# Optimization experiments

Measured on AMD Instinct MI355X. Metric: run time of the kernel, lower is better.

The kernel has to match this reference:

```python
import jax, jax.numpy as jnp
import numpy as np

B, S, D, H, DH = 2, 2048, 1024, 16, 64  # batch, seq, d_hidden, n_head, d_head


def setup_inputs() -> dict:
    key = jax.random.key(0)
    ks = jax.random.split(key, 11)
    sc = 0.02
    inp = {
        "Q": jax.random.normal(ks[0], (B, S, D), jnp.float32),
        "K": jax.random.normal(ks[1], (B, S, D), jnp.float32),
        "V": jax.random.normal(ks[2], (B, S, D), jnp.float32),
        # causal mask: True = masked (strictly upper triangular), broadcast to [B,S,S]
        "attn_mask": jnp.broadcast_to(jnp.triu(jnp.ones((S, S), bool), k=1), (B, S, S)),
        "W_q": jax.random.normal(ks[3], (H * DH, D), jnp.float32) * sc,
        "b_q": jnp.zeros((H * DH,), jnp.float32),
        "W_k": jax.random.normal(ks[4], (H * DH, D), jnp.float32) * sc,
        "b_k": jnp.zeros((H * DH,), jnp.float32),
        "W_v": jax.random.normal(ks[5], (H * DH, D), jnp.float32) * sc,
        "b_v": jnp.zeros((H * DH,), jnp.float32),
        "W_o": jax.random.normal(ks[6], (D, H * DH), jnp.float32) * sc,
        "b_o": jnp.zeros((D,), jnp.float32),
    }
    return inp


def reference(Q, K, V, attn_mask, W_q, b_q, W_k, b_k, W_v, b_v, W_o, b_o):
    scaler = 1.0 / (DH ** 0.5)
    # projections: torch Linear is x @ W.T + b
    def proj(x, W, b):
        y = jnp.einsum('bsd,ed->bse', x, W) + b  # e = H*DH
        return y.reshape(x.shape[0], x.shape[1], H, DH).transpose(0, 2, 1, 3)  # [B,H,S,DH]
    q = proj(Q, W_q, b_q)
    k = proj(K, W_k, b_k)
    v = proj(V, W_v, b_v)
    score = jnp.einsum('bhqd,bhkd->bhqk', q, k) * scaler
    score = jnp.where(attn_mask[:, None, :, :], jnp.float32(-1e9), score)
    attn_prob = jax.nn.softmax(score, axis=-1)  # dropout p=0.0 -> identity
    context = jnp.einsum('bhqk,bhkd->bhqd', attn_prob, v)
    context = context.transpose(0, 2, 1, 3).reshape(Q.shape[0], -1, H * DH)
    output = jnp.einsum('bse,de->bsd', context, W_o) + b_o
    return (output, attn_prob)
```

## Files before the change

kernel.cpp:

```cpp
#include <hip/hip_runtime.h>
#include <hip/hip_bf16.h>

typedef __attribute__((ext_vector_type(8))) __bf16 bf16x8;
typedef __attribute__((ext_vector_type(4))) float f32x4;
typedef __attribute__((ext_vector_type(4))) unsigned int u32x4;
typedef __attribute__((ext_vector_type(4))) float f4;

#define MB 2
#define MS 2048
#define MD 1024
#define MH 16
#define MDH 64

__device__ __forceinline__ void cvt_store16(const float* __restrict__ src, __bf16* dst) {
  f4 f0 = *(const f4*)src;
  f4 f1 = *(const f4*)(src + 4);
  f4 f2 = *(const f4*)(src + 8);
  f4 f3 = *(const f4*)(src + 12);
  bf16x8 lo, hi;
#pragma unroll
  for (int j = 0; j < 4; j++) {
    lo[j]     = (__bf16)f0[j];
    lo[j + 4] = (__bf16)f1[j];
    hi[j]     = (__bf16)f2[j];
    hi[j + 4] = (__bf16)f3[j];
  }
  *(bf16x8*)dst = lo;
  *(bf16x8*)(dst + 8) = hi;
}

template <bool ABF16>
__device__ __forceinline__ void gemm_core(const void* __restrict__ Aptr,
                                          const float* __restrict__ W,
                                          int tile_m, int tile_n,
                                          f32x4 acc[4][4]) {
  constexpr int LDT = 40;
  __shared__ __bf16 a_lds[128 * LDT];
  __shared__ __bf16 w_lds[128 * LDT];
  const int t = threadIdx.x;
  const int lane = t & 63;
  const int wave = t >> 6;
  const int l15 = lane & 15;
  const int quad = lane >> 4;
  const int wr = wave >> 1;
  const int wc = wave & 1;
  const int srow = t >> 1;
  const int scol = (t & 1) * 16;

  const f32x4 fzero = {0.f, 0.f, 0.f, 0.f};
#pragma unroll
  for (int mi = 0; mi < 4; mi++)
#pragma unroll
    for (int ni = 0; ni < 4; ni++) acc[mi][ni] = fzero;

  for (int k0 = 0; k0 < 1024; k0 += 32) {
    __syncthreads();
    if (ABF16) {
      const __bf16* A = (const __bf16*)Aptr;
      const __bf16* src = A + (size_t)(tile_m * 128 + srow) * 1024 + k0 + scol;
      u32x4 d0 = *(const u32x4*)src;
      u32x4 d1 = *(const u32x4*)(src + 8);
      *(u32x4*)&a_lds[srow * LDT + scol] = d0;
      *(u32x4*)&a_lds[srow * LDT + scol + 8] = d1;
    } else {
      const float* A = (const float*)Aptr;
      cvt_store16(A + (size_t)(tile_m * 128 + srow) * 1024 + k0 + scol,
                  &a_lds[srow * LDT + scol]);
    }
    cvt_store16(W + (size_t)(tile_n * 128 + srow) * 1024 + k0 + scol,
                &w_lds[srow * LDT + scol]);
    __syncthreads();

    bf16x8 af[4], bfr[4];
#pragma unroll
    for (int mi = 0; mi < 4; mi++)
      af[mi] = *(const bf16x8*)&a_lds[(wr * 64 + mi * 16 + l15) * LDT + quad * 8];
#pragma unroll
    for (int ni = 0; ni < 4; ni++)
      bfr[ni] = *(const bf16x8*)&w_lds[(wc * 64 + ni * 16 + l15) * LDT + quad * 8];
#pragma unroll
    for (int mi = 0; mi < 4; mi++)
#pragma unroll
      for (int ni = 0; ni < 4; ni++)
        acc[mi][ni] = __builtin_amdgcn_mfma_f32_16x16x32_bf16(af[mi], bfr[ni], acc[mi][ni], 0, 0, 0);
  }
}

__global__ __launch_bounds__(256) void qkv_proj(
    const float* __restrict__ Q, const float* __restrict__ K, const float* __restrict__ V,
    const float* __restrict__ Wq, const float* __restrict__ Wk, const float* __restrict__ Wv,
    const float* __restrict__ bq, const float* __restrict__ bk, const float* __restrict__ bv,
    __bf16* __restrict__ qo, __bf16* __restrict__ ko, __bf16* __restrict__ vo) {
  const int z = blockIdx.z;
  const float* A = (z == 0) ? Q : ((z == 1) ? K : V);
  const float* W = (z == 0) ? Wq : ((z == 1) ? Wk : Wv);
  const float* bias = (z == 0) ? bq : ((z == 1) ? bk : bv);
  __bf16* out = (z == 0) ? qo : ((z == 1) ? ko : vo);

  f32x4 acc[4][4];
  gemm_core<false>(A, W, blockIdx.y, blockIdx.x, acc);

  const int t = threadIdx.x;
  const int lane = t & 63, wave = t >> 6;
  const int l15 = lane & 15, quad = lane >> 4;
  const int wr = wave >> 1, wc = wave & 1;
  const float scale = (z == 0) ? 0.125f : 1.0f;

#pragma unroll
  for (int ni = 0; ni < 4; ni++) {
    const int e = blockIdx.x * 128 + wc * 64 + ni * 16 + l15;
    const float bias_v = bias[e];
    const int h = e >> 6, dh = e & 63;
#pragma unroll
    for (int mi = 0; mi < 4; mi++) {
#pragma unroll
      for (int r = 0; r < 4; r++) {
        const int sg = blockIdx.y * 128 + wr * 64 + mi * 16 + quad * 4 + r;
        const int bb = sg >> 11, s = sg & 2047;
        const float val = (acc[mi][ni][r] + bias_v) * scale;
        size_t addr;
        if (z < 2) addr = ((size_t)((bb * 16 + h) * 2048 + s)) * 64 + dh;
        else       addr = ((size_t)((bb * 16 + h) * 64 + dh)) * 2048 + s;
        out[addr] = (__bf16)val;
      }
    }
  }
}

__global__ __launch_bounds__(256) void attn_kernel(
    const __bf16* __restrict__ q, const __bf16* __restrict__ k,
    const __bf16* __restrict__ vt, float* __restrict__ P, __bf16* __restrict__ ctx) {
  const int qt = blockIdx.x, h = blockIdx.y, b = blockIdx.z;
  const int bh = b * 16 + h;
  const int t = threadIdx.x;
  const int lane = t & 63, wave = t >> 6;
  const int l15 = lane & 15, quad = lane >> 4;
  const int q0 = qt * 64;

  __shared__ __bf16 q_lds[64 * 72];
  __shared__ __bf16 k_lds[64 * 72];
  __shared__ __bf16 v_lds[64 * 72];
  __shared__ __bf16 p_lds[4 * 16 * 72];

  const __bf16* qbase = q + ((size_t)bh * 2048 + q0) * 64;
  const __bf16* kbase = k + (size_t)bh * 2048 * 64;
  const __bf16* vbase = vt + (size_t)bh * 64 * 2048;
  float* Pbase = P + ((size_t)bh * 2048 + q0) * 2048;

#pragma unroll
  for (int i = 0; i < 2; i++) {
    const int idx = t + i * 256;
    const int row = idx >> 3, c8 = (idx & 7) * 8;
    *(u32x4*)&q_lds[row * 72 + c8] = *(const u32x4*)(qbase + row * 64 + c8);
  }
  __syncthreads();
  bf16x8 qf[2];
  qf[0] = *(const bf16x8*)&q_lds[(wave * 16 + l15) * 72 + quad * 8];
  qf[1] = *(const bf16x8*)&q_lds[(wave * 16 + l15) * 72 + 32 + quad * 8];

  float m[4], l[4];
#pragma unroll
  for (int r = 0; r < 4; r++) { m[r] = -1e30f; l[r] = 0.f; }

  const f32x4 fzero = {0.f, 0.f, 0.f, 0.f};

  for (int kt = 0; kt <= qt; kt++) {
    __syncthreads();
#pragma unroll
    for (int i = 0; i < 2; i++) {
      const int idx = t + i * 256;
      const int row = idx >> 3, c8 = (idx & 7) * 8;
      *(u32x4*)&k_lds[row * 72 + c8] =
          *(const u32x4*)(kbase + (size_t)(kt * 64 + row) * 64 + c8);
    }
    __syncthreads();

    f32x4 sc[4];
#pragma unroll
    for (int blk = 0; blk < 4; blk++) {
      bf16x8 kf0 = *(const bf16x8*)&k_lds[(blk * 16 + l15) * 72 + quad * 8];
      bf16x8 kf1 = *(const bf16x8*)&k_lds[(blk * 16 + l15) * 72 + 32 + quad * 8];
      f32x4 zz = fzero;
      zz = __builtin_amdgcn_mfma_f32_16x16x32_bf16(qf[0], kf0, zz, 0, 0, 0);
      zz = __builtin_amdgcn_mfma_f32_16x16x32_bf16(qf[1], kf1, zz, 0, 0, 0);
      sc[blk] = zz;
    }
#pragma unroll
    for (int r = 0; r < 4; r++) {
      const int qrow = q0 + wave * 16 + quad * 4 + r;
      float sv[4];
      float rowmax = -1e30f;
#pragma unroll
      for (int blk = 0; blk < 4; blk++) {
        const int kcol = kt * 64 + blk * 16 + l15;
        float s = sc[blk][r];
        s = (kcol > qrow) ? -1e30f : s;
        sv[blk] = s;
        rowmax = fmaxf(rowmax, s);
      }
#pragma unroll
      for (int msk = 1; msk < 16; msk <<= 1)
        rowmax = fmaxf(rowmax, __shfl_xor(rowmax, msk, 64));
      const float mnew = fmaxf(m[r], rowmax);
      float se = 0.f;
#pragma unroll
      for (int blk = 0; blk < 4; blk++) se += __expf(sv[blk] - mnew);
#pragma unroll
      for (int msk = 1; msk < 16; msk <<= 1) se += __shfl_xor(se, msk, 64);
      l[r] = l[r] * __expf(m[r] - mnew) + se;
      m[r] = mnew;
    }
  }

  float rl[4];
#pragma unroll
  for (int r = 0; r < 4; r++) rl[r] = 1.0f / l[r];

  f32x4 o[4];
#pragma unroll
  for (int dblk = 0; dblk < 4; dblk++) o[dblk] = fzero;

  for (int kt = 0; kt < 32; kt++) {
    if (kt <= qt) {
      __syncthreads();
#pragma unroll
      for (int i = 0; i < 2; i++) {
        const int idx = t + i * 256;
        const int row = idx >> 3, c8 = (idx & 7) * 8;
        *(u32x4*)&k_lds[row * 72 + c8] =
            *(const u32x4*)(kbase + (size_t)(kt * 64 + row) * 64 + c8);
        *(u32x4*)&v_lds[row * 72 + c8] =
            *(const u32x4*)(vbase + (size_t)row * 2048 + kt * 64 + c8);
      }
      __syncthreads();

      f32x4 sc[4];
#pragma unroll
      for (int blk = 0; blk < 4; blk++) {
        bf16x8 kf0 = *(const bf16x8*)&k_lds[(blk * 16 + l15) * 72 + quad * 8];
        bf16x8 kf1 = *(const bf16x8*)&k_lds[(blk * 16 + l15) * 72 + 32 + quad * 8];
        f32x4 zz = fzero;
        zz = __builtin_amdgcn_mfma_f32_16x16x32_bf16(qf[0], kf0, zz, 0, 0, 0);
        zz = __builtin_amdgcn_mfma_f32_16x16x32_bf16(qf[1], kf1, zz, 0, 0, 0);
        sc[blk] = zz;
      }
#pragma unroll
      for (int r = 0; r < 4; r++) {
        const int qrow = q0 + wave * 16 + quad * 4 + r;
#pragma unroll
        for (int blk = 0; blk < 4; blk++) {
          const int kcol = kt * 64 + blk * 16 + l15;
          float s = sc[blk][r];
          s = (kcol > qrow) ? -1e30f : s;
          const float p = __expf(s - m[r]) * rl[r];
          Pbase[(size_t)(wave * 16 + quad * 4 + r) * 2048 + kcol] = p;
          p_lds[(wave * 16 + quad * 4 + r) * 72 + blk * 16 + l15] = (__bf16)p;
        }
      }
      bf16x8 pf0 = *(const bf16x8*)&p_lds[(wave * 16 + l15) * 72 + quad * 8];
      bf16x8 pf1 = *(const bf16x8*)&p_lds[(wave * 16 + l15) * 72 + 32 + quad * 8];
#pragma unroll
      for (int dblk = 0; dblk < 4; dblk++) {
        bf16x8 vf0 = *(const bf16x8*)&v_lds[(dblk * 16 + l15) * 72 + quad * 8];
        bf16x8 vf1 = *(const bf16x8*)&v_lds[(dblk * 16 + l15) * 72 + 32 + quad * 8];
        o[dblk] = __builtin_amdgcn_mfma_f32_16x16x32_bf16(pf0, vf0, o[dblk], 0, 0, 0);
        o[dblk] = __builtin_amdgcn_mfma_f32_16x16x32_bf16(pf1, vf1, o[dblk], 0, 0, 0);
      }
    } else {
#pragma unroll
      for (int r = 0; r < 4; r++)
#pragma unroll
        for (int blk = 0; blk < 4; blk++)
          Pbase[(size_t)(wave * 16 + quad * 4 + r) * 2048 + kt * 64 + blk * 16 + l15] = 0.f;
    }
  }

#pragma unroll
  for (int dblk = 0; dblk < 4; dblk++) {
#pragma unroll
    for (int r = 0; r < 4; r++) {
      const int sl = wave * 16 + quad * 4 + r;
      const size_t idx = ((size_t)(b * 2048 + q0 + sl)) * 1024 + h * 64 + dblk * 16 + l15;
      ctx[idx] = (__bf16)o[dblk][r];
    }
  }
}

__global__ __launch_bounds__(256) void out_proj(
    const __bf16* __restrict__ ctxp, const float* __restrict__ Wo,
    const float* __restrict__ bo, float* __restrict__ out) {
  f32x4 acc[4][4];
  gemm_core<true>(ctxp, Wo, blockIdx.y, blockIdx.x, acc);

  const int t = threadIdx.x;
  const int lane = t & 63, wave = t >> 6;
  const int l15 = lane & 15, quad = lane >> 4;
  const int wr = wave >> 1, wc = wave & 1;

#pragma unroll
  for (int ni = 0; ni < 4; ni++) {
    const int e = blockIdx.x * 128 + wc * 64 + ni * 16 + l15;
    const float bias_v = bo[e];
#pragma unroll
    for (int mi = 0; mi < 4; mi++) {
#pragma unroll
      for (int r = 0; r < 4; r++) {
        const int sg = blockIdx.y * 128 + wr * 64 + mi * 16 + quad * 4 + r;
        out[(size_t)sg * 1024 + e] = acc[mi][ni][r] + bias_v;
      }
    }
  }
}

extern "C" void kernel_launch(void* const* d_in, const int* in_sizes, int n_in,
                              void* d_out, int out_size, void* d_ws, size_t ws_size,
                              hipStream_t stream) {
  const float* Q  = (const float*)d_in[0];
  const float* K  = (const float*)d_in[1];
  const float* V  = (const float*)d_in[2];
  const float* Wq = (const float*)d_in[4];
  const float* bq = (const float*)d_in[5];
  const float* Wk = (const float*)d_in[6];
  const float* bk = (const float*)d_in[7];
  const float* Wv = (const float*)d_in[8];
  const float* bv = (const float*)d_in[9];
  const float* Wo = (const float*)d_in[10];
  const float* bo = (const float*)d_in[11];

  float* out0 = (float*)d_out;
  float* P = out0 + (size_t)MB * MS * MD;

  __bf16* qws = (__bf16*)d_ws;
  __bf16* kws = qws + (size_t)4194304;
  __bf16* vws = kws + (size_t)4194304;
  __bf16* cws = vws + (size_t)4194304;

  qkv_proj<<<dim3(8, 32, 3), 256, 0, stream>>>(Q, K, V, Wq, Wk, Wv, bq, bk, bv,
                                               qws, kws, vws);
  attn_kernel<<<dim3(32, 16, 2), 256, 0, stream>>>(qws, kws, vws, P, cws);
  out_proj<<<dim3(8, 32, 1), 256, 0, stream>>>(cws, Wo, bo, out0);
}
```

Measured before the change: 867.7 us.

## Pre-convert inputs to bf16, use direct global-to-LDS loads, restructure attention passes

Adds a separate kernel that converts Q/K/V and all weights to bf16 up front, so the GEMMs can stage tiles with global_load_lds into XOR-swizzled LDS using K=64 steps. The attention kernel's first pass now keeps per-lane running max/sum and merges across lanes only once at the end, processing two K tiles per sync. The masked upper region of P is zero-filled with vectorized stores instead of a per-tile loop. Query tiles are also launched heaviest-first to balance the causal work. The cost is an extra launch plus an extra round trip through memory for the converted activations, and more workspace.

Result: faster. 772.8 us (-10.9%).

```diff
diff --git a/kernel.cpp b/kernel.cpp
--- a/kernel.cpp
+++ b/kernel.cpp
@@ -3,7 +3,6 @@
 
 typedef __attribute__((ext_vector_type(8))) __bf16 bf16x8;
 typedef __attribute__((ext_vector_type(4))) float f32x4;
-typedef __attribute__((ext_vector_type(4))) unsigned int u32x4;
 typedef __attribute__((ext_vector_type(4))) float f4;
 
 #define MB 2
@@ -12,40 +11,69 @@
 #define MH 16
 #define MDH 64
 
-__device__ __forceinline__ void cvt_store16(const float* __restrict__ src, __bf16* dst) {
-  f4 f0 = *(const f4*)src;
-  f4 f1 = *(const f4*)(src + 4);
-  f4 f2 = *(const f4*)(src + 8);
-  f4 f3 = *(const f4*)(src + 12);
-  bf16x8 lo, hi;
+__device__ __forceinline__ void gl_lds16(const __bf16* g, __bf16* l) {
+  __builtin_amdgcn_global_load_lds(
+      (const __attribute__((address_space(1))) unsigned int*)g,
+      (__attribute__((address_space(3))) unsigned int*)l, 16, 0, 0);
+}
+
+__device__ __forceinline__ void stage64(const __bf16* __restrict__ g, int gstride,
+                                        __bf16* lds, int t) {
+#pragma unroll
+  for (int j = 0; j < 2; j++) {
+    const int slot = t + j * 256;
+    const int r = slot >> 3;
+    const int c = (slot & 7) ^ (r & 7);
+    gl_lds16(g + (size_t)r * gstride + c * 8, &lds[slot * 8]);
+  }
+}
+
+__device__ __forceinline__ bf16x8 frag_ld(const __bf16* lds, int row, int kc) {
+  const int slot = row * 8 + (kc ^ (row & 7));
+  return *(const bf16x8*)&lds[slot * 8];
+}
+
+__global__ __launch_bounds__(256) void convert_kernel(
+    const float* __restrict__ Q, const float* __restrict__ K, const float* __restrict__ V,
+    const float* __restrict__ Wq, const float* __restrict__ Wk, const float* __restrict__ Wv,
+    const float* __restrict__ Wo, __bf16* __restrict__ Ab, __bf16* __restrict__ Wb) {
+  const size_t base = ((size_t)blockIdx.x * 256 + threadIdx.x) * 8;
+  const float* src;
+  __bf16* dst;
+  size_t off;
+  if (base < 3UL * 4194304UL) {
+    const int z = (int)(base >> 22);
+    off = base & 4194303UL;
+    src = (z == 0) ? Q : ((z == 1) ? K : V);
+    dst = Ab + ((size_t)z << 22);
+  } else {
+    const size_t b2 = base - 3UL * 4194304UL;
+    const int w = (int)(b2 >> 20);
+    off = b2 & 1048575UL;
+    src = (w == 0) ? Wq : ((w == 1) ? Wk : ((w == 2) ? Wv : Wo));
+    dst = Wb + ((size_t)w << 20);
+  }
+  f4 a = *(const f4*)(src + off);
+  f4 b = *(const f4*)(src + off + 4);
+  bf16x8 o;
 #pragma unroll
   for (int j = 0; j < 4; j++) {
-    lo[j]     = (__bf16)f0[j];
-    lo[j + 4] = (__bf16)f1[j];
-    hi[j]     = (__bf16)f2[j];
-    hi[j + 4] = (__bf16)f3[j];
-  }
-  *(bf16x8*)dst = lo;
-  *(bf16x8*)(dst + 8) = hi;
-}
-
-template <bool ABF16>
-__device__ __forceinline__ void gemm_core(const void* __restrict__ Aptr,
-                                          const float* __restrict__ W,
+    o[j] = (__bf16)a[j];
+    o[j + 4] = (__bf16)b[j];
+  }
+  *(bf16x8*)(dst + off) = o;
+}
+
+__device__ __forceinline__ void gemm_core(const __bf16* __restrict__ A,
+                                          const __bf16* __restrict__ W,
                                           int tile_m, int tile_n,
                                           f32x4 acc[4][4]) {
-  constexpr int LDT = 40;
-  __shared__ __bf16 a_lds[128 * LDT];
-  __shared__ __bf16 w_lds[128 * LDT];
+  __shared__ __bf16 a_lds[8192];
+  __shared__ __bf16 w_lds[8192];
   const int t = threadIdx.x;
-  const int lane = t & 63;
-  const int wave = t >> 6;
-  const int l15 = lane & 15;
-  const int quad = lane >> 4;
-  const int wr = wave >> 1;
-  const int wc = wave & 1;
-  const int srow = t >> 1;
-  const int scol = (t & 1) * 16;
+  const int lane = t & 63, wave = t >> 6;
+  const int l15 = lane & 15, quad = lane >> 4;
+  const int wr = wave >> 1, wc = wave & 1;
 
   const f32x4 fzero = {0.f, 0.f, 0.f, 0.f};
 #pragma unroll
@@ -53,52 +81,57 @@
 #pragma unroll
     for (int ni = 0; ni < 4; ni++) acc[mi][ni] = fzero;
 
-  for (int k0 = 0; k0 < 1024; k0 += 32) {
-    __syncthreads();
-    if (ABF16) {
-      const __bf16* A = (const __bf16*)Aptr;
-      const __bf16* src = A + (size_t)(tile_m * 128 + srow) * 1024 + k0 + scol;
-      u32x4 d0 = *(const u32x4*)src;
-      u32x4 d1 = *(const u32x4*)(src + 8);
-      *(u32x4*)&a_lds[srow * LDT + scol] = d0;
-      *(u32x4*)&a_lds[srow * LDT + scol + 8] = d1;
-    } else {
-      const float* A = (const float*)Aptr;
-      cvt_store16(A + (size_t)(tile_m * 128 + srow) * 1024 + k0 + scol,
-                  &a_lds[srow * LDT + scol]);
-    }
-    cvt_store16(W + (size_t)(tile_n * 128 + srow) * 1024 + k0 + scol,
-                &w_lds[srow * LDT + scol]);
-    __syncthreads();
-
-    bf16x8 af[4], bfr[4];
-#pragma unroll
-    for (int mi = 0; mi < 4; mi++)
-      af[mi] = *(const bf16x8*)&a_lds[(wr * 64 + mi * 16 + l15) * LDT + quad * 8];
-#pragma unroll
-    for (int ni = 0; ni < 4; ni++)
-      bfr[ni] = *(const bf16x8*)&w_lds[(wc * 64 + ni * 16 + l15) * LDT + quad * 8];
-#pragma unroll
-    for (int mi = 0; mi < 4; mi++)
+  const __bf16* Abase = A + (size_t)(tile_m * 128) * 1024;
+  const __bf16* Wbase = W + (size_t)(tile_n * 128) * 1024;
+
+  for (int k0 = 0; k0 < 1024; k0 += 64) {
+    __syncthreads();
+#pragma unroll
+    for (int j = 0; j < 4; j++) {
+      const int slot = t + j * 256;
+      const int r = slot >> 3;
+      const int c = (slot & 7) ^ (r & 7);
+      gl_lds16(Abase + (size_t)r * 1024 + k0 + c * 8, &a_lds[slot * 8]);
+    }
+#pragma unroll
+    for (int j = 0; j < 4; j++) {
+      const int slot = t + j * 256;
+      const int r = slot >> 3;
+      const int c = (slot & 7) ^ (r & 7);
+      gl_lds16(Wbase + (size_t)r * 1024 + k0 + c * 8, &w_lds[slot * 8]);
+    }
+    __syncthreads();
+
+#pragma unroll
+    for (int kk = 0; kk < 2; kk++) {
+      bf16x8 af[4], bf[4];
+#pragma unroll
+      for (int mi = 0; mi < 4; mi++)
+        af[mi] = frag_ld(a_lds, wr * 64 + mi * 16 + l15, kk * 4 + quad);
 #pragma unroll
       for (int ni = 0; ni < 4; ni++)
-        acc[mi][ni] = __builtin_amdgcn_mfma_f32_16x16x32_bf16(af[mi], bfr[ni], acc[mi][ni], 0, 0, 0);
+        bf[ni] = frag_ld(w_lds, wc * 64 + ni * 16 + l15, kk * 4 + quad);
+#pragma unroll
+      for (int mi = 0; mi < 4; mi++)
+#pragma unroll
+        for (int ni = 0; ni < 4; ni++)
+          acc[mi][ni] = __builtin_amdgcn_mfma_f32_16x16x32_bf16(af[mi], bf[ni], acc[mi][ni], 0, 0, 0);
+    }
   }
 }
 
 __global__ __launch_bounds__(256) void qkv_proj(
-    const float* __restrict__ Q, const float* __restrict__ K, const float* __restrict__ V,
-    const float* __restrict__ Wq, const float* __restrict__ Wk, const float* __restrict__ Wv,
+    const __bf16* __restrict__ Ab, const __bf16* __restrict__ Wb,
     const float* __restrict__ bq, const float* __restrict__ bk, const float* __restrict__ bv,
     __bf16* __restrict__ qo, __bf16* __restrict__ ko, __bf16* __restrict__ vo) {
   const int z = blockIdx.z;
-  const float* A = (z == 0) ? Q : ((z == 1) ? K : V);
-  const float* W = (z == 0) ? Wq : ((z == 1) ? Wk : Wv);
+  const __bf16* A = Ab + ((size_t)z << 22);
+  const __bf16* W = Wb + ((size_t)z << 20);
   const float* bias = (z == 0) ? bq : ((z == 1) ? bk : bv);
   __bf16* out = (z == 0) ? qo : ((z == 1) ? ko : vo);
 
   f32x4 acc[4][4];
-  gemm_core<false>(A, W, blockIdx.y, blockIdx.x, acc);
+  gemm_core(A, W, blockIdx.y, blockIdx.x, acc);
 
   const int t = threadIdx.x;
   const int lane = t & 63, wave = t >> 6;
@@ -127,19 +160,57 @@
   }
 }
 
+__device__ __forceinline__ void qk_tile(const __bf16* kl, const bf16x8 qf0, const bf16x8 qf1,
+                                        int l15, int quad, f32x4 sc[4]) {
+  const f32x4 fzero = {0.f, 0.f, 0.f, 0.f};
+#pragma unroll
+  for (int blk = 0; blk < 4; blk++) {
+    bf16x8 kf0 = frag_ld(kl, blk * 16 + l15, quad);
+    bf16x8 kf1 = frag_ld(kl, blk * 16 + l15, 4 + quad);
+    f32x4 z = fzero;
+    z = __builtin_amdgcn_mfma_f32_16x16x32_bf16(qf0, kf0, z, 0, 0, 0);
+    z = __builtin_amdgcn_mfma_f32_16x16x32_bf16(qf1, kf1, z, 0, 0, 0);
+    sc[blk] = z;
+  }
+}
+
+__device__ __forceinline__ void sm_update(const f32x4 sc[4], int kt, int q0, int wave,
+                                          int quad, int l15, float m[4], float l[4]) {
+#pragma unroll
+  for (int r = 0; r < 4; r++) {
+    const int qrow = q0 + wave * 16 + quad * 4 + r;
+    float sv[4];
+    float nm = m[r];
+#pragma unroll
+    for (int blk = 0; blk < 4; blk++) {
+      const int kcol = kt * 64 + blk * 16 + l15;
+      float s = sc[blk][r];
+      s = (kcol > qrow) ? -1e30f : s;
+      sv[blk] = s;
+      nm = fmaxf(nm, s);
+    }
+    float acc = l[r] * __expf(m[r] - nm);
+#pragma unroll
+    for (int blk = 0; blk < 4; blk++) acc += __expf(sv[blk] - nm);
+    l[r] = acc;
+    m[r] = nm;
+  }
+}
+
 __global__ __launch_bounds__(256) void attn_kernel(
     const __bf16* __restrict__ q, const __bf16* __restrict__ k,
     const __bf16* __restrict__ vt, float* __restrict__ P, __bf16* __restrict__ ctx) {
-  const int qt = blockIdx.x, h = blockIdx.y, b = blockIdx.z;
+  const int qt = 31 - blockIdx.x;
+  const int h = blockIdx.y, b = blockIdx.z;
   const int bh = b * 16 + h;
   const int t = threadIdx.x;
   const int lane = t & 63, wave = t >> 6;
   const int l15 = lane & 15, quad = lane >> 4;
   const int q0 = qt * 64;
 
-  __shared__ __bf16 q_lds[64 * 72];
-  __shared__ __bf16 k_lds[64 * 72];
-  __shared__ __bf16 v_lds[64 * 72];
+  __shared__ __bf16 q_lds[4096];
+  __shared__ __bf16 k_lds[4096];
+  __shared__ __bf16 v_lds[4096];
   __shared__ __bf16 p_lds[4 * 16 * 72];
 
   const __bf16* qbase = q + ((size_t)bh * 2048 + q0) * 64;
@@ -147,150 +218,105 @@
   const __bf16* vbase = vt + (size_t)bh * 64 * 2048;
   float* Pbase = P + ((size_t)bh * 2048 + q0) * 2048;
 
-#pragma unroll
-  for (int i = 0; i < 2; i++) {
-    const int idx = t + i * 256;
-    const int row = idx >> 3, c8 = (idx & 7) * 8;
-    *(u32x4*)&q_lds[row * 72 + c8] = *(const u32x4*)(qbase + row * 64 + c8);
-  }
+  stage64(qbase, 64, q_lds, t);
   __syncthreads();
-  bf16x8 qf[2];
-  qf[0] = *(const bf16x8*)&q_lds[(wave * 16 + l15) * 72 + quad * 8];
-  qf[1] = *(const bf16x8*)&q_lds[(wave * 16 + l15) * 72 + 32 + quad * 8];
+  const bf16x8 qf0 = frag_ld(q_lds, wave * 16 + l15, quad);
+  const bf16x8 qf1 = frag_ld(q_lds, wave * 16 + l15, 4 + quad);
 
   float m[4], l[4];
 #pragma unroll
   for (int r = 0; r < 4; r++) { m[r] = -1e30f; l[r] = 0.f; }
 
+  for (int kt0 = 0; kt0 <= qt; kt0 += 2) {
+    const bool two = (kt0 + 1 <= qt);
+    __syncthreads();
+    stage64(kbase + (size_t)kt0 * 4096, 64, k_lds, t);
+    if (two) stage64(kbase + (size_t)(kt0 + 1) * 4096, 64, v_lds, t);
+    __syncthreads();
+    f32x4 sc[4];
+    qk_tile(k_lds, qf0, qf1, l15, quad, sc);
+    sm_update(sc, kt0, q0, wave, quad, l15, m, l);
+    if (two) {
+      qk_tile(v_lds, qf0, qf1, l15, quad, sc);
+      sm_update(sc, kt0 + 1, q0, wave, quad, l15, m, l);
+    }
+  }
+
+  float rl[4];
+#pragma unroll
+  for (int r = 0; r < 4; r++) {
+    float mm = m[r], ll = l[r];
+#pragma unroll
+    for (int msk = 1; msk < 16; msk <<= 1) {
+      const float mo = __shfl_xor(mm, msk, 64);
+      const float lo = __shfl_xor(ll, msk, 64);
+      const float mn = fmaxf(mm, mo);
+      ll = ll * __expf(mm - mn) + lo * __expf(mo - mn);
+      mm = mn;
+    }
+    m[r] = mm;
+    rl[r] = 1.0f / ll;
+  }
+
   const f32x4 fzero = {0.f, 0.f, 0.f, 0.f};
+  f32x4 o[4];
+#pragma unroll
+  for (int d = 0; d < 4; d++) o[d] = fzero;
 
   for (int kt = 0; kt <= qt; kt++) {
     __syncthreads();
-#pragma unroll
-    for (int i = 0; i < 2; i++) {
-      const int idx = t + i * 256;
-      const int row = idx >> 3, c8 = (idx & 7) * 8;
-      *(u32x4*)&k_lds[row * 72 + c8] =
-          *(const u32x4*)(kbase + (size_t)(kt * 64 + row) * 64 + c8);
-    }
+    stage64(kbase + (size_t)kt * 4096, 64, k_lds, t);
+    stage64(vbase + (size_t)kt * 64, 2048, v_lds, t);
     __syncthreads();
 
     f32x4 sc[4];
-#pragma unroll
-    for (int blk = 0; blk < 4; blk++) {
-      bf16x8 kf0 = *(const bf16x8*)&k_lds[(blk * 16 + l15) * 72 + quad * 8];
-      bf16x8 kf1 = *(const bf16x8*)&k_lds[(blk * 16 + l15) * 72 + 32 + quad * 8];
-      f32x4 zz = fzero;
-      zz = __builtin_amdgcn_mfma_f32_16x16x32_bf16(qf[0], kf0, zz, 0, 0, 0);
-      zz = __builtin_amdgcn_mfma_f32_16x16x32_bf16(qf[1], kf1, zz, 0, 0, 0);
-      sc[blk] = zz;
-    }
+    qk_tile(k_lds, qf0, qf1, l15, quad, sc);
+
 #pragma unroll
     for (int r = 0; r < 4; r++) {
       const int qrow = q0 + wave * 16 + quad * 4 + r;
-      float sv[4];
-      float rowmax = -1e30f;
 #pragma unroll
       for (int blk = 0; blk < 4; blk++) {
         const int kcol = kt * 64 + blk * 16 + l15;
         float s = sc[blk][r];
         s = (kcol > qrow) ? -1e30f : s;
-        sv[blk] = s;
-        rowmax = fmaxf(rowmax, s);
+        const float p = __expf(s - m[r]) * rl[r];
+        Pbase[(size_t)(wave * 16 + quad * 4 + r) * 2048 + kcol] = p;
+        p_lds[(wave * 16 + quad * 4 + r) * 72 + blk * 16 + l15] = (__bf16)p;
       }
-#pragma unroll
-      for (int msk = 1; msk < 16; msk <<= 1)
-        rowmax = fmaxf(rowmax, __shfl_xor(rowmax, msk, 64));
-      const float mnew = fmaxf(m[r], rowmax);
-      float se = 0.f;
-#pragma unroll
-      for (int blk = 0; blk < 4; blk++) se += __expf(sv[blk] - mnew);
-#pragma unroll
-      for (int msk = 1; msk < 16; msk <<= 1) se += __shfl_xor(se, msk, 64);
-      l[r] = l[r] * __expf(m[r] - mnew) + se;
-      m[r] = mnew;
-    }
-  }
-
-  float rl[4];
-#pragma unroll
-  for (int r = 0; r < 4; r++) rl[r] = 1.0f / l[r];
-
-  f32x4 o[4];
-#pragma unroll
-  for (int dblk = 0; dblk < 4; dblk++) o[dblk] = fzero;
-
-  for (int kt = 0; kt < 32; kt++) {
-    if (kt <= qt) {
-      __syncthreads();
-#pragma unroll
-      for (int i = 0; i < 2; i++) {
-        const int idx = t + i * 256;
-        const int row = idx >> 3, c8 = (idx & 7) * 8;
-        *(u32x4*)&k_lds[row * 72 + c8] =
-            *(const u32x4*)(kbase + (size_t)(kt * 64 + row) * 64 + c8);
-        *(u32x4*)&v_lds[row * 72 + c8] =
-            *(const u32x4*)(vbase + (size_t)row * 2048 + kt * 64 + c8);
-      }
-      __syncthreads();
-
-      f32x4 sc[4];
-#pragma unroll
-      for (int blk = 0; blk < 4; blk++) {
-        bf16x8 kf0 = *(const bf16x8*)&k_lds[(blk * 16 + l15) * 72 + quad * 8];
-        bf16x8 kf1 = *(const bf16x8*)&k_lds[(blk * 16 + l15) * 72 + 32 + quad * 8];
-        f32x4 zz = fzero;
-        zz = __builtin_amdgcn_mfma_f32_16x16x32_bf16(qf[0], kf0, zz, 0, 0, 0);
-        zz = __builtin_amdgcn_mfma_f32_16x16x32_bf16(qf[1], kf1, zz, 0, 0, 0);
-        sc[blk] = zz;
-      }
-#pragma unroll
-      for (int r = 0; r < 4; r++) {
-        const int qrow = q0 + wave * 16 + quad * 4 + r;
-#pragma unroll
-        for (int blk = 0; blk < 4; blk++) {
-          const int kcol = kt * 64 + blk * 16 + l15;
-          float s = sc[blk][r];
-          s = (kcol > qrow) ? -1e30f : s;
-          const float p = __expf(s - m[r]) * rl[r];
-          Pbase[(size_t)(wave * 16 + quad * 4 + r) * 2048 + kcol] = p;
-          p_lds[(wave * 16 + quad * 4 + r) * 72 + blk * 16 + l15] = (__bf16)p;
-        }
-      }
-      bf16x8 pf0 = *(const bf16x8*)&p_lds[(wave * 16 + l15) * 72 + quad * 8];
-      bf16x8 pf1 = *(const bf16x8*)&p_lds[(wave * 16 + l15) * 72 + 32 + quad * 8];
-#pragma unroll
-      for (int dblk = 0; dblk < 4; dblk++) {
-        bf16x8 vf0 = *(const bf16x8*)&v_lds[(dblk * 16 + l15) * 72 + quad * 8];
-        bf16x8 vf1 = *(const bf16x8*)&v_lds[(dblk * 16 + l15) * 72 + 32 + quad * 8];
-        o[dblk] = __builtin_amdgcn_mfma_f32_16x16x32_bf16(pf0, vf0, o[dblk], 0, 0, 0);
-        o[dblk] = __builtin_amdgcn_mfma_f32_16x16x32_bf16(pf1, vf1, o[dblk], 0, 0, 0);
-      }
-    } else {
-#pragma unroll
-      for (int r = 0; r < 4; r++)
-#pragma unroll
-        for (int blk = 0; blk < 4; blk++)
-          Pbase[(size_t)(wave * 16 + quad * 4 + r) * 2048 + kt * 64 + blk * 16 + l15] = 0.f;
-    }
-  }
-
-#pragma unroll
-  for (int dblk = 0; dblk < 4; dblk++) {
+    }
+    const bf16x8 pf0 = *(const bf16x8*)&p_lds[(wave * 16 + l15) * 72 + quad * 8];
+    const bf16x8 pf1 = *(const bf16x8*)&p_lds[(wave * 16 + l15) * 72 + 32 + quad * 8];
+#pragma unroll
+    for (int d = 0; d < 4; d++) {
+      bf16x8 vf0 = frag_ld(v_lds, d * 16 + l15, quad);
+      bf16x8 vf1 = frag_ld(v_lds, d * 16 + l15, 4 + quad);
+      o[d] = __builtin_amdgcn_mfma_f32_16x16x32_bf16(pf0, vf0, o[d], 0, 0, 0);
+      o[d] = __builtin_amdgcn_mfma_f32_16x16x32_bf16(pf1, vf1, o[d], 0, 0, 0);
+    }
+  }
+
+  const int c0 = (qt + 1) * 64;
+  const int zr = t >> 2;
+  for (int c = c0 + (t & 3) * 4; c < 2048; c += 16)
+    *(f32x4*)&Pbase[(size_t)zr * 2048 + c] = fzero;
+
+#pragma unroll
+  for (int d = 0; d < 4; d++) {
 #pragma unroll
     for (int r = 0; r < 4; r++) {
       const int sl = wave * 16 + quad * 4 + r;
-      const size_t idx = ((size_t)(b * 2048 + q0 + sl)) * 1024 + h * 64 + dblk * 16 + l15;
-      ctx[idx] = (__bf16)o[dblk][r];
+      const size_t idx = ((size_t)(b * 2048 + q0 + sl)) * 1024 + h * 64 + d * 16 + l15;
+      ctx[idx] = (__bf16)o[d][r];
     }
   }
 }
 
 __global__ __launch_bounds__(256) void out_proj(
-    const __bf16* __restrict__ ctxp, const float* __restrict__ Wo,
+    const __bf16* __restrict__ ctxp, const __bf16* __restrict__ Wob,
     const float* __restrict__ bo, float* __restrict__ out) {
   f32x4 acc[4][4];
-  gemm_core<true>(ctxp, Wo, blockIdx.y, blockIdx.x, acc);
+  gemm_core(ctxp, Wob, blockIdx.y, blockIdx.x, acc);
 
   const int t = threadIdx.x;
   const int lane = t & 63, wave = t >> 6;
@@ -330,13 +356,15 @@
   float* out0 = (float*)d_out;
   float* P = out0 + (size_t)MB * MS * MD;
 
-  __bf16* qws = (__bf16*)d_ws;
-  __bf16* kws = qws + (size_t)4194304;
-  __bf16* vws = kws + (size_t)4194304;
-  __bf16* cws = vws + (size_t)4194304;
-
-  qkv_proj<<<dim3(8, 32, 3), 256, 0, stream>>>(Q, K, V, Wq, Wk, Wv, bq, bk, bv,
-                                               qws, kws, vws);
+  __bf16* Ab  = (__bf16*)d_ws;
+  __bf16* Wb  = Ab + 3UL * 4194304UL;
+  __bf16* qws = Wb + 4UL * 1048576UL;
+  __bf16* kws = qws + 4194304UL;
+  __bf16* vws = kws + 4194304UL;
+  __bf16* cws = vws + 4194304UL;
+
+  convert_kernel<<<dim3(8192), 256, 0, stream>>>(Q, K, V, Wq, Wk, Wv, Wo, Ab, Wb);
+  qkv_proj<<<dim3(8, 32, 3), 256, 0, stream>>>(Ab, Wb, bq, bk, bv, qws, kws, vws);
   attn_kernel<<<dim3(32, 16, 2), 256, 0, stream>>>(qws, kws, vws, P, cws);
-  out_proj<<<dim3(8, 32, 1), 256, 0, stream>>>(cws, Wo, bo, out0);
-}
+  out_proj<<<dim3(8, 32, 1), 256, 0, stream>>>(cws, Wb + 3UL * 1048576UL, bo, out0);
+}
```
